# Kernel tuning notes

Hardware: AMD Instinct MI355X
Metric: run time of the kernel (lower is better)

Reference implementation:

```python
import jax, jax.numpy as jnp
import numpy as np

B = 512            # molecules
M = 24             # atoms per molecule
N = B * M          # total nodes
F = 128            # num_features
NRBF = 20          # num_rbf_features
CUTOFF = 5.0       # cutoff_dist
NUM_ATOM_TYPES = 100


def setup_inputs() -> dict:
    key = jax.random.key(0)
    ks = jax.random.split(key, 8)
    atoms = jax.random.randint(ks[0], (N,), 0, NUM_ATOM_TYPES, dtype=jnp.int64 if jax.config.jax_enable_x64 else jnp.int32)
    # positions in a ~6A box per molecule so many pairs fall under the 5A cutoff
    atom_positions = jax.random.uniform(ks[1], (N, 3), dtype=jnp.float32) * 6.0
    graph_indexes = jnp.repeat(jnp.arange(B), M)
    emb = jax.random.normal(ks[2], (NUM_ATOM_TYPES, F), dtype=jnp.float32)
    W1 = jax.random.normal(ks[3], (F, F), dtype=jnp.float32) / np.sqrt(F)
    b1 = jnp.zeros((F,), dtype=jnp.float32)
    W2 = jax.random.normal(ks[4], (F, 3 * F), dtype=jnp.float32) / np.sqrt(F)
    b2 = jnp.zeros((3 * F,), dtype=jnp.float32)
    Wf = jax.random.normal(ks[5], (NRBF, 3 * F), dtype=jnp.float32) / np.sqrt(NRBF)
    bf = jnp.zeros((3 * F,), dtype=jnp.float32)
    return {"atoms": atoms, "atom_positions": atom_positions, "graph_indexes": graph_indexes,
            "emb": emb, "W1": W1, "b1": b1, "W2": W2, "b2": b2, "Wf": Wf, "bf": bf}


def _painn_forward(atoms, atom_positions, emb, W1, b1, W2, b2, Wf, bf):
    # node embeddings s_i^0 and zero vector features v_i^0
    s = emb[atoms].reshape(B, M, F)                       # [B,M,F]
    v = jnp.zeros((B, M, F, 3), dtype=s.dtype)            # [B,M,F,3]
    pos = atom_positions.reshape(B, M, 3)

    # per-molecule dense neighbor list (same-molecule pairs within cutoff)
    r = pos[:, :, None, :] - pos[:, None, :, :]           # r_ij = pos_i - pos_j  [B,M,M,3]
    d = jnp.linalg.norm(r, axis=-1)                       # [B,M,M]
    mask = (d < CUTOFF) & ~jnp.eye(M, dtype=bool)         # exclude self (d=0 -> RBF div-by-zero)
    d_safe = jnp.where(mask, d, 1.0)

    # RBF: sin(n*pi*d/cutoff)/d, n = 1..20
    n = jnp.arange(1, NRBF + 1, dtype=s.dtype)
    rbf = jnp.sin(n * (jnp.pi / CUTOFF) * d_safe[..., None]) / d_safe[..., None]   # [B,M,M,20]
    Wedge = rbf @ Wf + bf                                 # edge filter  [B,M,M,3F]

    # node MLP phi(s_j): Linear(F,F) -> SiLU -> Linear(F,3F)
    phi = jax.nn.silu(s @ W1 + b1) @ W2 + b2              # [B,M,3F]

    # gather phi over j, modulate by edge filter, mask invalid edges
    msg = Wedge * phi[:, None, :, :] * mask[..., None]    # [B,M,M,3F]
    ds_m, dv_v, dv_r = jnp.split(msg, 3, axis=-1)         # each [B,M,M,F]

    ds = ds_m.sum(axis=2)                                 # scatter-sum over neighbors j -> [B,M,F]
    rhat = r / d_safe[..., None]                          # unit directions
    dv = (jnp.einsum('bijf,bjfc->bifc', dv_v, v)
          + jnp.einsum('bijf,bijc->bifc', dv_r, rhat))    # [B,M,F,3]

    s_new = s + ds
    v_new = v + dv
    return jnp.concatenate([s_new, v_new.reshape(B, M, 3 * F)], axis=-1)  # [B,M,4F]


def reference(atoms, atom_positions, graph_indexes, emb, W1, b1, W2, b2, Wf, bf):
    del graph_indexes  # batch structure is encoded by the fixed [B,M] layout
    return _painn_forward(atoms, atom_positions, emb, W1, b1, W2, b2, Wf, bf)
```

## Files before the change

kernel.cpp:

```cpp
#include <hip/hip_runtime.h>
#include <hip/hip_bf16.h>
#include <hip/hip_fp16.h>
#include <math.h>

#define B 512
#define M 24
#define F 128
#define NRBF 20
#define CUTOFF 5.0f
#define SA_LD 44


typedef __attribute__((ext_vector_type(8))) short short8;
typedef __attribute__((ext_vector_type(4))) float f32x4;

#define KIDX(g, e) ((((e) >> 2) << 4) + 4 * (g) + ((e) & 3))

__device__ __forceinline__ unsigned f2bf(float x) {
    unsigned u = __builtin_bit_cast(unsigned, x);
    return (u + 0x7FFFu + ((u >> 16) & 1u)) >> 16;
}
__device__ __forceinline__ unsigned f2h(float x) {
    __half h = __float2half(x);
    return (unsigned)__builtin_bit_cast(unsigned short, h);
}

__device__ __forceinline__ short8 pack_frag(unsigned u0, unsigned u1,
                                            unsigned u2, unsigned u3) {
    uint4 t = make_uint4(u0, u1, u2, u3);
    return __builtin_bit_cast(short8, t);
}

__device__ __forceinline__ short8 load_wfrag(const float* __restrict__ W, int ld,
                                             int col, int kbase, int kvalid, int g) {
    unsigned u[4];
#pragma unroll
    for (int q = 0; q < 4; ++q) {
        int k0 = kbase + KIDX(g, 2 * q);
        int k1 = kbase + KIDX(g, 2 * q + 1);
        float f0 = (k0 < kvalid) ? W[(size_t)k0 * ld + col] : 0.f;
        float f1 = (k1 < kvalid) ? W[(size_t)k1 * ld + col] : 0.f;
        u[q] = f2bf(f0) | (f2bf(f1) << 16);
    }
    return pack_frag(u[0], u[1], u[2], u[3]);
}

__device__ __forceinline__ short8 load_wffrag(const float* __restrict__ Wf,
                                              const float* __restrict__ bfv,
                                              int col, int g) {
    unsigned u[4];
#pragma unroll
    for (int q = 0; q < 4; ++q) {
        int k0 = KIDX(g, 2 * q);
        int k1 = KIDX(g, 2 * q + 1);
        float f0 = (k0 < NRBF) ? Wf[(size_t)k0 * (3 * F) + col]
                               : (k0 == NRBF ? bfv[col] : 0.f);
        float f1 = (k1 < NRBF) ? Wf[(size_t)k1 * (3 * F) + col]
                               : (k1 == NRBF ? bfv[col] : 0.f);
        u[q] = f2bf(f0) | (f2bf(f1) << 16);
    }
    return pack_frag(u[0], u[1], u[2], u[3]);
}

__device__ __forceinline__ short8 load_afrag(const short* sp, int row, int ldsh,
                                             int kbase, int g) {
    const short* p = sp + row * ldsh + kbase + 4 * g;
    uint2 lo = *(const uint2*)(p);
    uint2 hi = *(const uint2*)(p + 16);
    return pack_frag(lo.x, lo.y, hi.x, hi.y);
}

__global__ __launch_bounds__(512, 2) void painn_kernel(
    const int* __restrict__ atoms,
    const float* __restrict__ apos,
    const float* __restrict__ emb,
    const float* __restrict__ W1, const float* __restrict__ b1,
    const float* __restrict__ W2, const float* __restrict__ b2,
    const float* __restrict__ Wf, const float* __restrict__ bf,
    float* __restrict__ out)
{
    __shared__ __attribute__((aligned(16))) short sH[32 * 136];
    __shared__ __attribute__((aligned(16))) float sPhi[32][F][2];
    __shared__ __attribute__((aligned(16))) short sA[8 * 32 * SA_LD];
    __shared__ __attribute__((aligned(16))) short sGeoH[8 * 32 * 4];
    __shared__ __attribute__((aligned(16))) float sPos[M][4];

    const int tid  = threadIdx.x;
    const int b    = blockIdx.x;
    const int wid  = tid >> 6;
    const int lane = tid & 63;
    const int g    = lane >> 4;
    const int lrow = lane & 15;
    const int f2   = wid * 16 + lrow;

    for (int idx = tid; idx < M * (F / 4); idx += 512) {
        int node = idx >> 5;
        int f4 = idx & 31;
        int a = atoms[b * M + node];
        float4 v = reinterpret_cast<const float4*>(emb + (size_t)a * F)[f4];
        unsigned u0 = f2bf(v.x) | (f2bf(v.y) << 16);
        unsigned u1 = f2bf(v.z) | (f2bf(v.w) << 16);
        *reinterpret_cast<uint2*>(&sH[node * 136 + f4 * 4]) = make_uint2(u0, u1);
    }
    for (int t = tid; t < 544; t += 512)
        reinterpret_cast<unsigned*>(sH)[24 * 68 + t] = 0u;
    if (tid < M * 3) sPos[tid / 3][tid % 3] = apos[(size_t)b * M * 3 + tid];
    __syncthreads();

    {
        float b1v = b1[f2];
        f32x4 c[2] = {{0.f, 0.f, 0.f, 0.f}, {0.f, 0.f, 0.f, 0.f}};
#pragma unroll
        for (int ks = 0; ks < 4; ++ks) {
            short8 bfrag = load_wfrag(W1, F, f2, ks * 32, 128, g);
            short8 a0 = load_afrag(sH, lrow, 136, ks * 32, g);
            short8 a1 = load_afrag(sH, 16 + lrow, 136, ks * 32, g);
            c[0] = __builtin_amdgcn_mfma_f32_16x16x32_bf16(a0, bfrag, c[0], 0, 0, 0);
            c[1] = __builtin_amdgcn_mfma_f32_16x16x32_bf16(a1, bfrag, c[1], 0, 0, 0);
        }
        __syncthreads();
#pragma unroll
        for (int rt = 0; rt < 2; ++rt)
#pragma unroll
            for (int r = 0; r < 4; ++r) {
                int row = rt * 16 + g * 4 + r;
                float x = c[rt][r] + b1v;
                float h = x / (1.0f + __expf(-x));
                sH[row * 136 + f2] = (short)f2bf(h);
            }
    }
    __syncthreads();

#pragma unroll
    for (int half = 0; half < 2; ++half) {
        int wcol = half ? (256 + f2) : f2;
        float b2v = b2[wcol];
        f32x4 c[2] = {{0.f, 0.f, 0.f, 0.f}, {0.f, 0.f, 0.f, 0.f}};
#pragma unroll
        for (int ks = 0; ks < 4; ++ks) {
            short8 bfrag = load_wfrag(W2, 3 * F, wcol, ks * 32, 128, g);
            short8 a0 = load_afrag(sH, lrow, 136, ks * 32, g);
            short8 a1 = load_afrag(sH, 16 + lrow, 136, ks * 32, g);
            c[0] = __builtin_amdgcn_mfma_f32_16x16x32_bf16(a0, bfrag, c[0], 0, 0, 0);
            c[1] = __builtin_amdgcn_mfma_f32_16x16x32_bf16(a1, bfrag, c[1], 0, 0, 0);
        }
#pragma unroll
        for (int rt = 0; rt < 2; ++rt)
#pragma unroll
            for (int r = 0; r < 4; ++r) {
                int row = rt * 16 + g * 4 + r;
                sPhi[row][f2][half] = c[rt][r] + b2v;
            }
    }
    __syncthreads();

    short8 wfrag0 = load_wffrag(Wf, bf, f2, g);
    short8 wfrag2 = load_wffrag(Wf, bf, 256 + f2, g);
    const float kth = 3.14159265358979323846f / CUTOFF;

    float ph0[8], ph2[8];
#pragma unroll
    for (int rt = 0; rt < 2; ++rt)
#pragma unroll
        for (int r = 0; r < 4; ++r) {
            int j = rt * 16 + g * 4 + r;
            ph0[rt * 4 + r] = sPhi[j][f2][0];
            ph2[rt * 4 + r] = sPhi[j][f2][1];
        }

    for (int ic = 0; ic < 3; ++ic) {
        if (tid < 256) {
            int il = tid >> 5, j = tid & 31;
            int i = ic * 8 + il;
            unsigned pk[16];
#pragma unroll
            for (int q = 0; q < 16; ++q) pk[q] = 0u;
            unsigned gxy = 0u, gz = 0u;
            if (j < M && j != i) {
                float dx = sPos[i][0] - sPos[j][0];
                float dy = sPos[i][1] - sPos[j][1];
                float dz = sPos[i][2] - sPos[j][2];
                float d = sqrtf(dx * dx + dy * dy + dz * dz);
                if (d < CUTOFF) {
                    float inv = 1.0f / d;
                    float s1, c1;
                    __sincosf(kth * d, &s1, &c1);
                    float cc = 2.0f * c1;
                    float vp = s1 * inv;
                    float vc = 2.0f * s1 * c1 * inv;
                    pk[0] = f2bf(vp) | (f2bf(vc) << 16);
#pragma unroll
                    for (int q = 1; q < 10; ++q) {
                        float v3 = cc * vc - vp;
                        float v4 = cc * v3 - vc;
                        pk[q] = f2bf(v3) | (f2bf(v4) << 16);
                        vp = v3; vc = v4;
                    }
                    pk[10] = 0x3F80u;
                    gxy = f2h(dx * inv) | (f2h(dy * inv) << 16);
                    gz  = f2h(dz * inv);
                }
            }
            short* rp = &sA[(il * 32 + j) * SA_LD];
#pragma unroll
            for (int q = 0; q < 8; ++q)
                *reinterpret_cast<uint2*>(rp + q * 4) = make_uint2(pk[2 * q], pk[2 * q + 1]);
            *reinterpret_cast<uint2*>(&sGeoH[(il * 32 + j) * 4]) = make_uint2(gxy, gz);
        }
        __syncthreads();

        for (int il = 0; il < 8; ++il) {
            const int i = ic * 8 + il;
            float s0 = 0.f, ax = 0.f, ay = 0.f, az = 0.f;
#pragma unroll
            for (int rt = 0; rt < 2; ++rt) {
                short8 afr = load_afrag(sA, il * 32 + rt * 16 + lrow, SA_LD, 0, g);
                f32x4 z4 = {0.f, 0.f, 0.f, 0.f};
                f32x4 c0 = __builtin_amdgcn_mfma_f32_16x16x32_bf16(afr, wfrag0, z4, 0, 0, 0);
                f32x4 c2 = __builtin_amdgcn_mfma_f32_16x16x32_bf16(afr, wfrag2, z4, 0, 0, 0);
#pragma unroll
                for (int r = 0; r < 4; ++r) {
                    int j = rt * 16 + g * 4 + r;
                    uint2 gw = *reinterpret_cast<const uint2*>(&sGeoH[(il * 32 + j) * 4]);
                    float2 xy = __half22float2(__builtin_bit_cast(__half2, gw.x));
                    float gzf = __half2float(__builtin_bit_cast(__half2, gw.y).x);
                    s0 = fmaf(c0[r], ph0[rt * 4 + r], s0);
                    float m2 = c2[r] * ph2[rt * 4 + r];
                    ax = fmaf(m2, xy.x, ax);
                    ay = fmaf(m2, xy.y, ay);
                    az = fmaf(m2, gzf, az);
                }
            }
            s0 += __shfl_xor(s0, 16); s0 += __shfl_xor(s0, 32);
            ax += __shfl_xor(ax, 16); ax += __shfl_xor(ax, 32);
            ay += __shfl_xor(ay, 16); ay += __shfl_xor(ay, 32);
            az += __shfl_xor(az, 16); az += __shfl_xor(az, 32);
            if (lane < 16) {
                const int node = b * M + i;
                const int a = atoms[node];
                float embv = emb[(size_t)a * F + f2];
                float* o = out + (size_t)node * (4 * F);
                o[f2] = embv + s0;
                o[F + 3 * f2 + 0] = ax;
                o[F + 3 * f2 + 1] = ay;
                o[F + 3 * f2 + 2] = az;
            }
        }
        __syncthreads();
    }
}

extern "C" void kernel_launch(void* const* d_in, const int* in_sizes, int n_in,
                              void* d_out, int out_size, void* d_ws, size_t ws_size,
                              hipStream_t stream) {
    const int*   atoms = (const int*)d_in[0];
    const float* apos  = (const float*)d_in[1];
    const float* emb = (const float*)d_in[3];
    const float* W1  = (const float*)d_in[4];
    const float* b1  = (const float*)d_in[5];
    const float* W2  = (const float*)d_in[6];
    const float* b2  = (const float*)d_in[7];
    const float* Wf  = (const float*)d_in[8];
    const float* bf  = (const float*)d_in[9];
    float* out = (float*)d_out;

    painn_kernel<<<B, 512, 0, stream>>>(atoms, apos, emb, W1, b1, W2, b2, Wf, bf, out);
}
```

Measured before the change: 36.12 us.

## Prepack bf16 weight fragments in a pre-kernel and double-buffer edge tiles

A small pack kernel converts W1, W2, Wf+bias and the embedding table to bf16 once per call, already laid out in MFMA fragment order in the workspace. Each block then loads a fragment with a single uint4 read instead of eight strided fp32 reads plus conversion, repeated across all 512 blocks. The main kernel also keeps phi in registers rather than round-tripping through shared memory. It double-buffers the RBF/geometry tiles so the next chunk is built while the current one is consumed, and stores geometry as float4 instead of fp16. The cost is an extra kernel launch and more shared memory for the double buffers.

```diff
diff --git a/kernel.cpp b/kernel.cpp
--- a/kernel.cpp
+++ b/kernel.cpp
@@ -1,6 +1,5 @@
 #include <hip/hip_runtime.h>
 #include <hip/hip_bf16.h>
-#include <hip/hip_fp16.h>
 #include <math.h>
 
 #define B 512
@@ -9,6 +8,8 @@
 #define NRBF 20
 #define CUTOFF 5.0f
 #define SA_LD 44
+#define SH_LD 140
+#define CHUNK 8
 
 
 typedef __attribute__((ext_vector_type(8))) short short8;
@@ -20,46 +21,60 @@
     unsigned u = __builtin_bit_cast(unsigned, x);
     return (u + 0x7FFFu + ((u >> 16) & 1u)) >> 16;
 }
-__device__ __forceinline__ unsigned f2h(float x) {
-    __half h = __float2half(x);
-    return (unsigned)__builtin_bit_cast(unsigned short, h);
-}
-
-__device__ __forceinline__ short8 pack_frag(unsigned u0, unsigned u1,
-                                            unsigned u2, unsigned u3) {
-    uint4 t = make_uint4(u0, u1, u2, u3);
-    return __builtin_bit_cast(short8, t);
-}
-
-__device__ __forceinline__ short8 load_wfrag(const float* __restrict__ W, int ld,
-                                             int col, int kbase, int kvalid, int g) {
-    unsigned u[4];
-#pragma unroll
-    for (int q = 0; q < 4; ++q) {
-        int k0 = kbase + KIDX(g, 2 * q);
-        int k1 = kbase + KIDX(g, 2 * q + 1);
-        float f0 = (k0 < kvalid) ? W[(size_t)k0 * ld + col] : 0.f;
-        float f1 = (k1 < kvalid) ? W[(size_t)k1 * ld + col] : 0.f;
-        u[q] = f2bf(f0) | (f2bf(f1) << 16);
-    }
-    return pack_frag(u[0], u[1], u[2], u[3]);
-}
-
-__device__ __forceinline__ short8 load_wffrag(const float* __restrict__ Wf,
-                                              const float* __restrict__ bfv,
-                                              int col, int g) {
-    unsigned u[4];
-#pragma unroll
-    for (int q = 0; q < 4; ++q) {
-        int k0 = KIDX(g, 2 * q);
-        int k1 = KIDX(g, 2 * q + 1);
-        float f0 = (k0 < NRBF) ? Wf[(size_t)k0 * (3 * F) + col]
-                               : (k0 == NRBF ? bfv[col] : 0.f);
-        float f1 = (k1 < NRBF) ? Wf[(size_t)k1 * (3 * F) + col]
-                               : (k1 == NRBF ? bfv[col] : 0.f);
-        u[q] = f2bf(f0) | (f2bf(f1) << 16);
-    }
-    return pack_frag(u[0], u[1], u[2], u[3]);
+
+#define WS_W2 2048
+#define WS_WF 6144
+#define WS_EMB 7168
+
+__global__ void pack_kernel(const float* __restrict__ W1,
+                            const float* __restrict__ W2,
+                            const float* __restrict__ Wf,
+                            const float* __restrict__ bf,
+                            const float* __restrict__ emb,
+                            uint4* __restrict__ ws) {
+    int idx = blockIdx.x * 256 + threadIdx.x;
+    if (idx < 2048) {
+        int f2 = idx & 127, g = (idx >> 7) & 3, ks = idx >> 9;
+        unsigned u[4];
+#pragma unroll
+        for (int q = 0; q < 4; ++q) {
+            int k0 = ks * 32 + KIDX(g, 2 * q);
+            int k1 = ks * 32 + KIDX(g, 2 * q + 1);
+            u[q] = f2bf(W1[(size_t)k0 * F + f2]) | (f2bf(W1[(size_t)k1 * F + f2]) << 16);
+        }
+        ws[idx] = make_uint4(u[0], u[1], u[2], u[3]);
+    } else if (idx < 6144) {
+        int t = idx - 2048;
+        int f2 = t & 127, g = (t >> 7) & 3, ks = (t >> 9) & 3, half = t >> 11;
+        int col = half ? 256 + f2 : f2;
+        unsigned u[4];
+#pragma unroll
+        for (int q = 0; q < 4; ++q) {
+            int k0 = ks * 32 + KIDX(g, 2 * q);
+            int k1 = ks * 32 + KIDX(g, 2 * q + 1);
+            u[q] = f2bf(W2[(size_t)k0 * (3 * F) + col]) | (f2bf(W2[(size_t)k1 * (3 * F) + col]) << 16);
+        }
+        ws[idx] = make_uint4(u[0], u[1], u[2], u[3]);
+    } else if (idx < 7168) {
+        int t = idx - 6144;
+        int f2 = t & 127, g = (t >> 7) & 3, half = t >> 9;
+        int col = half ? 256 + f2 : f2;
+        unsigned u[4];
+#pragma unroll
+        for (int q = 0; q < 4; ++q) {
+            int k0 = KIDX(g, 2 * q);
+            int k1 = KIDX(g, 2 * q + 1);
+            float f0 = (k0 < NRBF) ? Wf[(size_t)k0 * (3 * F) + col] : (k0 == NRBF ? bf[col] : 0.f);
+            float f1 = (k1 < NRBF) ? Wf[(size_t)k1 * (3 * F) + col] : (k1 == NRBF ? bf[col] : 0.f);
+            u[q] = f2bf(f0) | (f2bf(f1) << 16);
+        }
+        ws[idx] = make_uint4(u[0], u[1], u[2], u[3]);
+    } else if (idx < 7168 + 3200) {
+        int t = idx - 7168;
+        float4 v = reinterpret_cast<const float4*>(emb)[t];
+        uint2 o = make_uint2(f2bf(v.x) | (f2bf(v.y) << 16), f2bf(v.z) | (f2bf(v.w) << 16));
+        reinterpret_cast<uint2*>(ws + WS_EMB)[t] = o;
+    }
 }
 
 __device__ __forceinline__ short8 load_afrag(const short* sp, int row, int ldsh,
@@ -67,22 +82,22 @@
     const short* p = sp + row * ldsh + kbase + 4 * g;
     uint2 lo = *(const uint2*)(p);
     uint2 hi = *(const uint2*)(p + 16);
-    return pack_frag(lo.x, lo.y, hi.x, hi.y);
+    uint4 t = make_uint4(lo.x, lo.y, hi.x, hi.y);
+    return __builtin_bit_cast(short8, t);
 }
 
 __global__ __launch_bounds__(512, 2) void painn_kernel(
     const int* __restrict__ atoms,
     const float* __restrict__ apos,
     const float* __restrict__ emb,
-    const float* __restrict__ W1, const float* __restrict__ b1,
-    const float* __restrict__ W2, const float* __restrict__ b2,
-    const float* __restrict__ Wf, const float* __restrict__ bf,
-    float* __restrict__ out)
+    const float* __restrict__ b1,
+    const float* __restrict__ b2,
+    float* __restrict__ out,
+    const uint4* __restrict__ ws)
 {
-    __shared__ __attribute__((aligned(16))) short sH[32 * 136];
-    __shared__ __attribute__((aligned(16))) float sPhi[32][F][2];
-    __shared__ __attribute__((aligned(16))) short sA[8 * 32 * SA_LD];
-    __shared__ __attribute__((aligned(16))) short sGeoH[8 * 32 * 4];
+    __shared__ __attribute__((aligned(16))) short sH[32 * SH_LD];
+    __shared__ __attribute__((aligned(16))) short sA[2][CHUNK * 32 * SA_LD];
+    __shared__ __attribute__((aligned(16))) float4 sGeo[2][CHUNK * 32];
     __shared__ __attribute__((aligned(16))) float sPos[M][4];
 
     const int tid  = threadIdx.x;
@@ -93,17 +108,18 @@
     const int lrow = lane & 15;
     const int f2   = wid * 16 + lrow;
 
-    for (int idx = tid; idx < M * (F / 4); idx += 512) {
+    const short* pEmb = reinterpret_cast<const short*>(ws + WS_EMB);
+    const float kth = 3.14159265358979323846f / CUTOFF;
+
+    for (int idx = tid; idx < M * 32; idx += 512) {
         int node = idx >> 5;
         int f4 = idx & 31;
         int a = atoms[b * M + node];
-        float4 v = reinterpret_cast<const float4*>(emb + (size_t)a * F)[f4];
-        unsigned u0 = f2bf(v.x) | (f2bf(v.y) << 16);
-        unsigned u1 = f2bf(v.z) | (f2bf(v.w) << 16);
-        *reinterpret_cast<uint2*>(&sH[node * 136 + f4 * 4]) = make_uint2(u0, u1);
-    }
-    for (int t = tid; t < 544; t += 512)
-        reinterpret_cast<unsigned*>(sH)[24 * 68 + t] = 0u;
+        uint2 v = *reinterpret_cast<const uint2*>(pEmb + (size_t)a * F + f4 * 4);
+        *reinterpret_cast<uint2*>(&sH[node * SH_LD + f4 * 4]) = v;
+    }
+    for (int t = tid; t < 560; t += 512)
+        reinterpret_cast<unsigned*>(sH)[1680 + t] = 0u;
     if (tid < M * 3) sPos[tid / 3][tid % 3] = apos[(size_t)b * M * 3 + tid];
     __syncthreads();
 
@@ -112,9 +128,9 @@
         f32x4 c[2] = {{0.f, 0.f, 0.f, 0.f}, {0.f, 0.f, 0.f, 0.f}};
 #pragma unroll
         for (int ks = 0; ks < 4; ++ks) {
-            short8 bfrag = load_wfrag(W1, F, f2, ks * 32, 128, g);
-            short8 a0 = load_afrag(sH, lrow, 136, ks * 32, g);
-            short8 a1 = load_afrag(sH, 16 + lrow, 136, ks * 32, g);
+            short8 bfrag = __builtin_bit_cast(short8, ws[(ks * 4 + g) * 128 + f2]);
+            short8 a0 = load_afrag(sH, lrow, SH_LD, ks * 32, g);
+            short8 a1 = load_afrag(sH, 16 + lrow, SH_LD, ks * 32, g);
             c[0] = __builtin_amdgcn_mfma_f32_16x16x32_bf16(a0, bfrag, c[0], 0, 0, 0);
             c[1] = __builtin_amdgcn_mfma_f32_16x16x32_bf16(a1, bfrag, c[1], 0, 0, 0);
         }
@@ -126,21 +142,22 @@
                 int row = rt * 16 + g * 4 + r;
                 float x = c[rt][r] + b1v;
                 float h = x / (1.0f + __expf(-x));
-                sH[row * 136 + f2] = (short)f2bf(h);
+                sH[row * SH_LD + f2] = (short)f2bf(h);
             }
     }
     __syncthreads();
 
+    float ph0[8], ph2[8];
 #pragma unroll
     for (int half = 0; half < 2; ++half) {
-        int wcol = half ? (256 + f2) : f2;
-        float b2v = b2[wcol];
+        float b2v = b2[half ? (256 + f2) : f2];
         f32x4 c[2] = {{0.f, 0.f, 0.f, 0.f}, {0.f, 0.f, 0.f, 0.f}};
 #pragma unroll
         for (int ks = 0; ks < 4; ++ks) {
-            short8 bfrag = load_wfrag(W2, 3 * F, wcol, ks * 32, 128, g);
-            short8 a0 = load_afrag(sH, lrow, 136, ks * 32, g);
-            short8 a1 = load_afrag(sH, 16 + lrow, 136, ks * 32, g);
+            short8 bfrag = __builtin_bit_cast(short8,
+                ws[WS_W2 + ((half * 4 + ks) * 4 + g) * 128 + f2]);
+            short8 a0 = load_afrag(sH, lrow, SH_LD, ks * 32, g);
+            short8 a1 = load_afrag(sH, 16 + lrow, SH_LD, ks * 32, g);
             c[0] = __builtin_amdgcn_mfma_f32_16x16x32_bf16(a0, bfrag, c[0], 0, 0, 0);
             c[1] = __builtin_amdgcn_mfma_f32_16x16x32_bf16(a1, bfrag, c[1], 0, 0, 0);
         }
@@ -148,87 +165,82 @@
         for (int rt = 0; rt < 2; ++rt)
 #pragma unroll
             for (int r = 0; r < 4; ++r) {
-                int row = rt * 16 + g * 4 + r;
-                sPhi[row][f2][half] = c[rt][r] + b2v;
-            }
-    }
+                if (half == 0) ph0[rt * 4 + r] = c[rt][r] + b2v;
+                else           ph2[rt * 4 + r] = c[rt][r] + b2v;
+            }
+    }
+
+    short8 wfrag0 = __builtin_bit_cast(short8, ws[WS_WF + (0 * 4 + g) * 128 + f2]);
+    short8 wfrag2 = __builtin_bit_cast(short8, ws[WS_WF + (1 * 4 + g) * 128 + f2]);
+
+    const int pil = tid >> 5;
+    const int pj  = tid & 31;
+
+    unsigned pk[16];
+    float4 g4;
+
+    auto produce = [&](int ic) {
+#pragma unroll
+        for (int q = 0; q < 16; ++q) pk[q] = 0u;
+        g4 = make_float4(0.f, 0.f, 0.f, 0.f);
+        int i = ic * CHUNK + pil;
+        if (pj < M && pj != i) {
+            float dx = sPos[i][0] - sPos[pj][0];
+            float dy = sPos[i][1] - sPos[pj][1];
+            float dz = sPos[i][2] - sPos[pj][2];
+            float d = sqrtf(dx * dx + dy * dy + dz * dz);
+            if (d < CUTOFF) {
+                float inv = 1.0f / d;
+                float s1, c1;
+                __sincosf(kth * d, &s1, &c1);
+                float cc = 2.0f * c1;
+                float vp = s1 * inv;
+                float vc = 2.0f * s1 * c1 * inv;
+                pk[0] = f2bf(vp) | (f2bf(vc) << 16);
+#pragma unroll
+                for (int q = 1; q < 10; ++q) {
+                    float v3 = cc * vc - vp;
+                    float v4 = cc * v3 - vc;
+                    pk[q] = f2bf(v3) | (f2bf(v4) << 16);
+                    vp = v3; vc = v4;
+                }
+                pk[10] = 0x3F80u;
+                g4 = make_float4(dx * inv, dy * inv, dz * inv, 1.f);
+            }
+        }
+    };
+    auto writebuf = [&](int buf) {
+        short* rp = &sA[buf][(pil * 32 + pj) * SA_LD];
+#pragma unroll
+        for (int q = 0; q < 8; ++q)
+            *reinterpret_cast<uint2*>(rp + q * 4) = make_uint2(pk[2 * q], pk[2 * q + 1]);
+        sGeo[buf][pil * 32 + pj] = g4;
+    };
+
+    if (tid < 256) { produce(0); writebuf(0); }
     __syncthreads();
 
-    short8 wfrag0 = load_wffrag(Wf, bf, f2, g);
-    short8 wfrag2 = load_wffrag(Wf, bf, 256 + f2, g);
-    const float kth = 3.14159265358979323846f / CUTOFF;
-
-    float ph0[8], ph2[8];
-#pragma unroll
-    for (int rt = 0; rt < 2; ++rt)
-#pragma unroll
-        for (int r = 0; r < 4; ++r) {
-            int j = rt * 16 + g * 4 + r;
-            ph0[rt * 4 + r] = sPhi[j][f2][0];
-            ph2[rt * 4 + r] = sPhi[j][f2][1];
-        }
-
     for (int ic = 0; ic < 3; ++ic) {
-        if (tid < 256) {
-            int il = tid >> 5, j = tid & 31;
-            int i = ic * 8 + il;
-            unsigned pk[16];
-#pragma unroll
-            for (int q = 0; q < 16; ++q) pk[q] = 0u;
-            unsigned gxy = 0u, gz = 0u;
-            if (j < M && j != i) {
-                float dx = sPos[i][0] - sPos[j][0];
-                float dy = sPos[i][1] - sPos[j][1];
-                float dz = sPos[i][2] - sPos[j][2];
-                float d = sqrtf(dx * dx + dy * dy + dz * dz);
-                if (d < CUTOFF) {
-                    float inv = 1.0f / d;
-                    float s1, c1;
-                    __sincosf(kth * d, &s1, &c1);
-                    float cc = 2.0f * c1;
-                    float vp = s1 * inv;
-                    float vc = 2.0f * s1 * c1 * inv;
-                    pk[0] = f2bf(vp) | (f2bf(vc) << 16);
-#pragma unroll
-                    for (int q = 1; q < 10; ++q) {
-                        float v3 = cc * vc - vp;
-                        float v4 = cc * v3 - vc;
-                        pk[q] = f2bf(v3) | (f2bf(v4) << 16);
-                        vp = v3; vc = v4;
-                    }
-                    pk[10] = 0x3F80u;
-                    gxy = f2h(dx * inv) | (f2h(dy * inv) << 16);
-                    gz  = f2h(dz * inv);
-                }
-            }
-            short* rp = &sA[(il * 32 + j) * SA_LD];
-#pragma unroll
-            for (int q = 0; q < 8; ++q)
-                *reinterpret_cast<uint2*>(rp + q * 4) = make_uint2(pk[2 * q], pk[2 * q + 1]);
-            *reinterpret_cast<uint2*>(&sGeoH[(il * 32 + j) * 4]) = make_uint2(gxy, gz);
-        }
-        __syncthreads();
-
-        for (int il = 0; il < 8; ++il) {
-            const int i = ic * 8 + il;
+        const int buf = ic & 1;
+        if (ic < 2 && tid < 256) { produce(ic + 1); writebuf(buf ^ 1); }
+        for (int il = 0; il < CHUNK; ++il) {
+            const int i = ic * CHUNK + il;
             float s0 = 0.f, ax = 0.f, ay = 0.f, az = 0.f;
 #pragma unroll
             for (int rt = 0; rt < 2; ++rt) {
-                short8 afr = load_afrag(sA, il * 32 + rt * 16 + lrow, SA_LD, 0, g);
+                short8 afr = load_afrag(&sA[buf][0], il * 32 + rt * 16 + lrow, SA_LD, 0, g);
                 f32x4 z4 = {0.f, 0.f, 0.f, 0.f};
                 f32x4 c0 = __builtin_amdgcn_mfma_f32_16x16x32_bf16(afr, wfrag0, z4, 0, 0, 0);
                 f32x4 c2 = __builtin_amdgcn_mfma_f32_16x16x32_bf16(afr, wfrag2, z4, 0, 0, 0);
 #pragma unroll
                 for (int r = 0; r < 4; ++r) {
                     int j = rt * 16 + g * 4 + r;
-                    uint2 gw = *reinterpret_cast<const uint2*>(&sGeoH[(il * 32 + j) * 4]);
-                    float2 xy = __half22float2(__builtin_bit_cast(__half2, gw.x));
-                    float gzf = __half2float(__builtin_bit_cast(__half2, gw.y).x);
+                    float4 ge = sGeo[buf][il * 32 + j];
                     s0 = fmaf(c0[r], ph0[rt * 4 + r], s0);
                     float m2 = c2[r] * ph2[rt * 4 + r];
-                    ax = fmaf(m2, xy.x, ax);
-                    ay = fmaf(m2, xy.y, ay);
-                    az = fmaf(m2, gzf, az);
+                    ax = fmaf(m2, ge.x, ax);
+                    ay = fmaf(m2, ge.y, ay);
+                    az = fmaf(m2, ge.z, az);
                 }
             }
             s0 += __shfl_xor(s0, 16); s0 += __shfl_xor(s0, 32);
@@ -238,9 +250,8 @@
             if (lane < 16) {
                 const int node = b * M + i;
                 const int a = atoms[node];
-                float embv = emb[(size_t)a * F + f2];
                 float* o = out + (size_t)node * (4 * F);
-                o[f2] = embv + s0;
+                o[f2] = emb[(size_t)a * F + f2] + s0;
                 o[F + 3 * f2 + 0] = ax;
                 o[F + 3 * f2 + 1] = ay;
                 o[F + 3 * f2 + 2] = az;
@@ -263,6 +274,8 @@
     const float* Wf  = (const float*)d_in[8];
     const float* bf  = (const float*)d_in[9];
     float* out = (float*)d_out;
-
-    painn_kernel<<<B, 512, 0, stream>>>(atoms, apos, emb, W1, b1, W2, b2, Wf, bf, out);
-}
+    uint4* ws = (uint4*)d_ws;
+
+    pack_kernel<<<41, 256, 0, stream>>>(W1, W2, Wf, bf, emb, ws);
+    painn_kernel<<<B, 512, 0, stream>>>(atoms, apos, emb, b1, b2, out, ws);
+}
```

Measured after the change: 41.31 us. 14.4% more time.
